# Optimization experiments

Measured on AMD Instinct MI355X. Metric: run time of the kernel, lower is better.

## Reference

```python
import jax, jax.numpy as jnp
import numpy as np

NUM_TOKEN = 16  # number of joint tokens; each locally-connected position has its own weights


def setup_inputs() -> dict:
    key = jax.random.key(0)
    k1, k2, k3 = jax.random.split(key, 3)
    b, n = 64, 256
    input_size, ff_size, output_size = 2048, 8192, 2048
    T = NUM_TOKEN
    cin, cff, cout = input_size // T, ff_size // T, output_size // T
    x = jax.random.normal(k1, (b, n, input_size), dtype=jnp.float32)
    # LocallyConnected2d weights: independent [out_ch, in_ch] matrix per token position t
    w1 = jax.random.normal(k2, (cff, cin, T), dtype=jnp.float32) * 0.05
    w2 = jax.random.normal(k3, (cout, cff, T), dtype=jnp.float32) * 0.05
    return {"x": x, "w1": w1, "w2": w2}


def reference(x, w1, w2):
    # x: [b, n, f]; reshape(b*n, f//T, T) matches torch's reshape(b*n, f//T, T, 1)
    b, n, f = x.shape
    T = NUM_TOKEN
    xr = x.reshape(b * n, f // T, T)  # [B, Cin, T]
    # LocallyConnected2d with k=1: per-position channel mixing (unfold degenerates to identity)
    h = jnp.einsum('bct,oct->bot', xr, w1)          # [B, Cff, T]
    h = jax.nn.gelu(h, approximate=False)           # nn.GELU default is exact erf form
    # dropout is identity in eval / deterministic reference
    y = jnp.einsum('bct,oct->bot', h, w2)           # [B, Cout, T]
    return y.reshape(b, n, -1)                      # feature index = o*T + t, same as torch
```

## Files before the change

kernel.cpp:

```cpp
#include <hip/hip_runtime.h>
#include <hip/hip_bf16.h>
#include <math.h>


typedef __attribute__((ext_vector_type(8))) short bf16x8;
typedef __attribute__((ext_vector_type(4))) float f32x4;

#define MFMA16(a,b,c) __builtin_amdgcn_mfma_f32_16x16x32_bf16((a),(b),(c),0,0,0)

#define N_ROWS   16384
#define XT_PLANE (16384*128)
#define W_TSTR   65536
#define W_JSTR   16384

static __device__ __forceinline__ unsigned short f2bf(float f){
  union{float f; unsigned u;} v; v.f = f;
  return (unsigned short)((v.u + 0x7FFFu + ((v.u>>16)&1u))>>16);
}
static __device__ __forceinline__ unsigned cvtpk(float lo, float hi){
  unsigned r;
  asm("v_cvt_pk_bf16_f32 %0, %1, %2" : "=v"(r) : "v"(lo), "v"(hi));
  return r;
}
static __device__ __forceinline__ float bflo(unsigned u){
  union{unsigned x; float f;} c; c.x = u<<16; return c.f;
}
static __device__ __forceinline__ float bfhi(unsigned u){
  union{unsigned x; float f;} c; c.x = u & 0xffff0000u; return c.f;
}
static __device__ __forceinline__ float gelu_fast(float x){
  float x2 = x*x;
  float m  = x*(-1.5957691216f - 0.0713548163f*x2);
  float e  = __expf(m);
  return x*__builtin_amdgcn_rcpf(1.0f + e);
}

typedef __attribute__((address_space(1))) const unsigned int gas_u32;
typedef __attribute__((address_space(3))) unsigned int las_u32;
static __device__ __forceinline__ void gload16(const void* g, void* l){
  __builtin_amdgcn_global_load_lds((gas_u32*)g, (las_u32*)l, 16, 0, 0);
}
static __device__ __forceinline__ unsigned lds_off(const void* p){
  return (unsigned)(size_t)(const __attribute__((address_space(3))) void*)p;
}

__global__ __launch_bounds__(256) void k_packw(const float* __restrict__ w1,
                                               const float* __restrict__ w2,
                                               unsigned short* __restrict__ w1p,
                                               unsigned short* __restrict__ w2p){
  int g = blockIdx.x*256 + threadIdx.x;
  bool is1 = (g < 131072);
  int gg = is1 ? g : (g - 131072);
  int l  = gg & 63, q = (l>>4), i = l & 15;
  int ks = (gg>>6)&3, m8 = (gg>>8)&7, jc = (gg>>11)&3, t = (gg>>13)&15;
  union { unsigned short s[8]; bf16x8 v; } u;
  if (is1){
    int o  = jc*128 + m8*16 + i;
    int c0 = ks*32 + q*8;
    #pragma unroll
    for (int j=0;j<8;++j) u.s[j] = f2bf(w1[(o*128 + c0 + j)*16 + t]);
    *(bf16x8*)(w1p + (size_t)gg*8) = u.v;
  } else {
    int o2  = m8*16 + i;
    int cf0 = jc*128 + ks*32 + q*8;
    #pragma unroll
    for (int j=0;j<8;++j) u.s[j] = f2bf(w2[(o2*512 + cf0 + j)*16 + t]);
    *(bf16x8*)(w2p + (size_t)gg*8) = u.v;
  }
}

#define TRRD(d, a, OFS) asm volatile("ds_read_b64_tr_b16 %0, %1 offset:" OFS \
                                     : "=v"(d) : "v"(a))
__global__ __launch_bounds__(256) void k_xt(const float* __restrict__ x,
                                            unsigned short* __restrict__ xt){
  __shared__ unsigned short ls[8*2048];
  const int r0 = blockIdx.x*8;
  const int tid = threadIdx.x;
  #pragma unroll
  for (int it=0; it<16; ++it){
    int idx = it*256 + tid;
    int row = idx>>9, rem = idx&511;
    float4 v = *(const float4*)(x + (size_t)(r0+row)*2048 + rem*4);
    unsigned lo = cvtpk(v.x, v.y), hi = cvtpk(v.z, v.w);
    unsigned long long p = ((unsigned long long)hi<<32) | lo;
    *(unsigned long long*)(ls + row*2048 + rem*4) = p;
  }
  __syncthreads();
  const int wv = tid>>6, l = tid&63, g = l>>4, i = l&15;
  unsigned base = lds_off(ls) + (unsigned)wv*8192u + (unsigned)l*8u;
  #pragma unroll
  for (int rr=0; rr<2; ++rr){
    unsigned long long d0,d1,d2,d3,d4,d5,d6,d7;
    if (rr==0){
      TRRD(d0, base, "0");    TRRD(d1, base, "512");
      TRRD(d2, base, "1024"); TRRD(d3, base, "1536");
      TRRD(d4, base, "2048"); TRRD(d5, base, "2560");
      TRRD(d6, base, "3072"); TRRD(d7, base, "3584");
    } else {
      TRRD(d0, base, "4096"); TRRD(d1, base, "4608");
      TRRD(d2, base, "5120"); TRRD(d3, base, "5632");
      TRRD(d4, base, "6144"); TRRD(d5, base, "6656");
      TRRD(d6, base, "7168"); TRRD(d7, base, "7680");
    }
    asm volatile("s_waitcnt lgkmcnt(0)" ::: "memory");
    __builtin_amdgcn_sched_barrier(0);
    unsigned short* xp = xt + (size_t)i*XT_PLANE
                       + (size_t)(r0 + 2*wv + rr)*128 + g*4;
    *(unsigned long long*)(xp + 0*16)  = d0;
    *(unsigned long long*)(xp + 1*16)  = d1;
    *(unsigned long long*)(xp + 2*16)  = d2;
    *(unsigned long long*)(xp + 3*16)  = d3;
    *(unsigned long long*)(xp + 4*16)  = d4;
    *(unsigned long long*)(xp + 5*16)  = d5;
    *(unsigned long long*)(xp + 6*16)  = d6;
    *(unsigned long long*)(xp + 7*16)  = d7;
  }
}

__global__ __launch_bounds__(256,2) void k_ffn(const unsigned short* __restrict__ xt,
                                               const unsigned short* __restrict__ w1p,
                                               const unsigned short* __restrict__ w2p,
                                               unsigned short* __restrict__ yt){
  __shared__ unsigned short ws[2*16384];
  const int bx = blockIdx.x;
  const int t = bx>>7, rt = bx&127, r0 = rt<<7;
  const int tid = threadIdx.x;
  const int wv = tid>>6, l = tid&63, q = l>>4, i = l&15;

  const unsigned short* w1t = w1p + (size_t)t*W_TSTR;
  const unsigned short* w2t = w2p + (size_t)t*W_TSTR;

  auto stage = [&](int hc, int buf){
    const int jc = hc>>1, half = hc&1;
    const unsigned short* w1c = w1t + jc*W_JSTR + half*8192;
    const unsigned short* w2c = w2t + jc*W_JSTR + half*1024;
    unsigned short* Wb = ws + buf*16384;
    #pragma unroll
    for (int c=0;c<8;++c){
      int k = wv*8 + c;
      if (k < 16){
        gload16(w1c + k*512 + l*8, Wb + k*512 + l*8);
      } else {
        int f = k - 16;
        gload16(w2c + (f>>1)*2048 + (f&1)*512 + l*8, Wb + 8192 + f*512 + l*8);
      }
    }
  };

  stage(0, 0);

  bf16x8 xb[4][2];
  {
    const unsigned short* xp = xt + (size_t)t*XT_PLANE + (size_t)(r0 + wv*32)*128;
    #pragma unroll
    for (int ks=0; ks<4; ++ks){
      xb[ks][0] = *(const bf16x8*)(xp + (size_t)i*128 + ks*32 + q*8);
      xb[ks][1] = *(const bf16x8*)(xp + (size_t)(i+16)*128 + ks*32 + q*8);
    }
  }
  __syncthreads();

  f32x4 accY[2][8];
  #pragma unroll
  for (int a=0;a<2;++a)
    #pragma unroll
    for (int b=0;b<8;++b) accY[a][b] = (f32x4){0.f,0.f,0.f,0.f};

  const int idxA = ((q&1)*32 + i)*4;
  const int idxB = idxA + 64;
  const int lo32 = (l < 32);

  int cur = 0;
  #pragma unroll 1
  for (int hc=0; hc<8; ++hc){
    if (hc < 7) stage(hc+1, cur^1);

    const unsigned short* W1 = ws + cur*16384;
    const unsigned short* W2 = W1 + 8192;

    f32x4 acc1[4][2];
    #pragma unroll
    for (int a=0;a<4;++a){ acc1[a][0]=(f32x4){0,0,0,0}; acc1[a][1]=(f32x4){0,0,0,0}; }
    #pragma unroll
    for (int ks=0; ks<4; ++ks){
      #pragma unroll
      for (int mt=0; mt<4; ++mt){
        bf16x8 af = *(const bf16x8*)(W1 + (mt*4+ks)*512 + l*8);
        acc1[mt][0] = MFMA16(af, xb[ks][0], acc1[mt][0]);
        acc1[mt][1] = MFMA16(af, xb[ks][1], acc1[mt][1]);
      }
    }

    unsigned pk[4][2][2];
    #pragma unroll
    for (int mt=0; mt<4; ++mt)
      #pragma unroll
      for (int nt=0; nt<2; ++nt){
        f32x4 v = acc1[mt][nt];
        pk[mt][nt][0] = cvtpk(gelu_fast(v.x), gelu_fast(v.y));
        pk[mt][nt][1] = cvtpk(gelu_fast(v.z), gelu_fast(v.w));
      }

    #pragma unroll
    for (int ks2=0; ks2<2; ++ks2){
      bf16x8 a2[2];
      #pragma unroll
      for (int nt=0; nt<2; ++nt){
        int pA0=(int)pk[2*ks2  ][nt][0], pA1=(int)pk[2*ks2  ][nt][1];
        int pB0=(int)pk[2*ks2+1][nt][0], pB1=(int)pk[2*ks2+1][nt][1];
        int a0 = __builtin_amdgcn_ds_bpermute(idxA, pA0);
        int b0 = __builtin_amdgcn_ds_bpermute(idxA, pB0);
        int a1 = __builtin_amdgcn_ds_bpermute(idxA, pA1);
        int b1 = __builtin_amdgcn_ds_bpermute(idxA, pB1);
        int a2r= __builtin_amdgcn_ds_bpermute(idxB, pA0);
        int b2 = __builtin_amdgcn_ds_bpermute(idxB, pB0);
        int a3 = __builtin_amdgcn_ds_bpermute(idxB, pA1);
        int b3 = __builtin_amdgcn_ds_bpermute(idxB, pB1);
        union{ int ii[4]; bf16x8 v; } u;
        u.ii[0] = lo32 ? a0 : b0;
        u.ii[1] = lo32 ? a1 : b1;
        u.ii[2] = lo32 ? a2r: b2;
        u.ii[3] = lo32 ? a3 : b3;
        a2[nt] = u.v;
      }
      #pragma unroll
      for (int nt2=0; nt2<8; ++nt2){
        bf16x8 bf = *(const bf16x8*)(W2 + (nt2*2+ks2)*512 + l*8);
        accY[0][nt2] = MFMA16(a2[0], bf, accY[0][nt2]);
        accY[1][nt2] = MFMA16(a2[1], bf, accY[1][nt2]);
      }
    }

    __syncthreads();
    cur ^= 1;
  }

  unsigned short* yp = yt + (size_t)t*XT_PLANE + (size_t)(r0 + wv*32)*128;
  #pragma unroll
  for (int mt2=0; mt2<2; ++mt2)
    #pragma unroll
    for (int nt2=0; nt2<8; ++nt2){
      f32x4 v = accY[mt2][nt2];
      unsigned p01 = cvtpk(v.x, v.y);
      unsigned p23 = cvtpk(v.z, v.w);
      int o = nt2*16 + i;
      int rowb = mt2*16 + q*4;
      yp[(rowb+0)*128 + o] = (unsigned short)(p01 & 0xffffu);
      yp[(rowb+1)*128 + o] = (unsigned short)(p01 >> 16);
      yp[(rowb+2)*128 + o] = (unsigned short)(p23 & 0xffffu);
      yp[(rowb+3)*128 + o] = (unsigned short)(p23 >> 16);
    }
}

__global__ __launch_bounds__(256) void k_out(const unsigned short* __restrict__ yt,
                                             float* __restrict__ out){
  const int r0 = blockIdx.x*8;
  const int tid = threadIdx.x;
  const int r = tid>>5, w = tid&31;
  const int og = w&15, tq0 = w>>4;
  #pragma unroll
  for (int it=0; it<2; ++it){
    int tq = tq0 + it*2;
    const unsigned short* yp = yt + (size_t)(tq*4)*XT_PLANE
                             + (size_t)(r0+r)*128 + og*8;
    union{ bf16x8 v; unsigned u[4]; } y0, y1, y2, y3;
    y0.v = *(const bf16x8*)(yp);
    y1.v = *(const bf16x8*)(yp + XT_PLANE);
    y2.v = *(const bf16x8*)(yp + 2*XT_PLANE);
    y3.v = *(const bf16x8*)(yp + 3*XT_PLANE);
    float* op = out + (size_t)(r0+r)*2048 + og*128 + tq*4;
    #pragma unroll
    for (int k=0;k<8;++k){
      unsigned w0 = y0.u[k>>1], w1 = y1.u[k>>1], w2 = y2.u[k>>1], w3 = y3.u[k>>1];
      f32x4 o4;
      if (k&1){ o4.x=bfhi(w0); o4.y=bfhi(w1); o4.z=bfhi(w2); o4.w=bfhi(w3); }
      else    { o4.x=bflo(w0); o4.y=bflo(w1); o4.z=bflo(w2); o4.w=bflo(w3); }
      *(f32x4*)(op + k*16) = o4;
    }
  }
}

__global__ __launch_bounds__(128) void k_naive(const float* __restrict__ x,
                                               const float* __restrict__ w1,
                                               const float* __restrict__ w2,
                                               float* __restrict__ out){
  int bid = blockIdx.x; int t = bid & 15; int row = bid >> 4;
  int tid = threadIdx.x;
  __shared__ float xsm[128]; __shared__ float hsm[512];
  xsm[tid] = x[(size_t)row*2048 + tid*16 + t];
  __syncthreads();
  for (int kk=0; kk<4; ++kk){
    int o = kk*128 + tid; float a = 0.f;
    for (int c=0;c<128;++c) a += xsm[c]*w1[(o*128+c)*16+t];
    hsm[o] = 0.5f*a*(1.0f+erff(a*0.70710678f));
  }
  __syncthreads();
  float a = 0.f;
  for (int cf=0; cf<512; ++cf) a += hsm[cf]*w2[(tid*512+cf)*16+t];
  out[(size_t)row*2048 + tid*16 + t] = a;
}

extern "C" void kernel_launch(void* const* d_in, const int* in_sizes, int n_in,
                              void* d_out, int out_size, void* d_ws, size_t ws_size,
                              hipStream_t stream){
  const float* x  = (const float*)d_in[0];
  const float* w1 = (const float*)d_in[1];
  const float* w2 = (const float*)d_in[2];
  float* out = (float*)d_out;

  const size_t NEEDED = 71303168ULL;
  if (ws_size < NEEDED || d_ws == nullptr){
    k_naive<<<dim3(16384*16), dim3(128), 0, stream>>>(x, w1, w2, out);
    return;
  }
  unsigned short* xt  = (unsigned short*)d_ws;
  unsigned short* w1p = xt + 33554432;
  unsigned short* w2p = w1p + 1048576;

  k_packw<<<dim3(1024), dim3(256), 0, stream>>>(w1, w2, w1p, w2p);
  k_xt  <<<dim3(2048), dim3(256), 0, stream>>>(x, xt);
  k_ffn <<<dim3(2048), dim3(256), 0, stream>>>(xt, w1p, w2p, xt);
  k_out <<<dim3(2048), dim3(256), 0, stream>>>(xt, out);
}
```

Before: 404.1 us.

## Coalesce transpose stores via LDS and shrink FFN weight stage for 3 blocks/CU

The x-transpose kernel now stages transposed data back through LDS, so it can write full 16-byte coalesced rows to the per-token planes instead of scattered 8-byte stores. The FFN kernel halves its per-iteration weight chunk (16 smaller stages instead of 8) and cuts LDS use so three blocks fit per CU. Its epilogue stages output through padded LDS before issuing vector stores. The output kernel now gathers the bf16 planes into LDS and uses transpose reads to write contiguous fp32 rows. The smaller FFN chunks mean more barriers and more stage overhead, traded against higher occupancy and better-coalesced global traffic.

```diff
diff --git a/kernel.cpp b/kernel.cpp
--- a/kernel.cpp
+++ b/kernel.cpp
@@ -22,11 +22,8 @@
   asm("v_cvt_pk_bf16_f32 %0, %1, %2" : "=v"(r) : "v"(lo), "v"(hi));
   return r;
 }
-static __device__ __forceinline__ float bflo(unsigned u){
-  union{unsigned x; float f;} c; c.x = u<<16; return c.f;
-}
-static __device__ __forceinline__ float bfhi(unsigned u){
-  union{unsigned x; float f;} c; c.x = u & 0xffff0000u; return c.f;
+static __device__ __forceinline__ float bfs(unsigned short s){
+  union{unsigned u; float f;} c; c.u = ((unsigned)s)<<16; return c.f;
 }
 static __device__ __forceinline__ float gelu_fast(float x){
   float x2 = x*x;
@@ -73,7 +70,7 @@
                                      : "=v"(d) : "v"(a))
 __global__ __launch_bounds__(256) void k_xt(const float* __restrict__ x,
                                             unsigned short* __restrict__ xt){
-  __shared__ unsigned short ls[8*2048];
+  __shared__ unsigned short ls[16512];
   const int r0 = blockIdx.x*8;
   const int tid = threadIdx.x;
   #pragma unroll
@@ -84,6 +81,191 @@
     unsigned lo = cvtpk(v.x, v.y), hi = cvtpk(v.z, v.w);
     unsigned long long p = ((unsigned long long)hi<<32) | lo;
     *(unsigned long long*)(ls + row*2048 + rem*4) = p;
+  }
+  __syncthreads();
+  const int wv = tid>>6, l = tid&63, g = l>>4, i = l&15;
+  unsigned base = lds_off(ls) + (unsigned)wv*8192u + (unsigned)l*8u;
+  unsigned long long d[16];
+  TRRD(d[0],  base, "0");    TRRD(d[1],  base, "512");
+  TRRD(d[2],  base, "1024"); TRRD(d[3],  base, "1536");
+  TRRD(d[4],  base, "2048"); TRRD(d[5],  base, "2560");
+  TRRD(d[6],  base, "3072"); TRRD(d[7],  base, "3584");
+  TRRD(d[8],  base, "4096"); TRRD(d[9],  base, "4608");
+  TRRD(d[10], base, "5120"); TRRD(d[11], base, "5632");
+  TRRD(d[12], base, "6144"); TRRD(d[13], base, "6656");
+  TRRD(d[14], base, "7168"); TRRD(d[15], base, "7680");
+  asm volatile("s_waitcnt lgkmcnt(0)" ::: "memory");
+  __builtin_amdgcn_sched_barrier(0);
+  __syncthreads();
+  #pragma unroll
+  for (int rr=0; rr<2; ++rr)
+    #pragma unroll
+    for (int ch=0; ch<8; ++ch)
+      *(unsigned long long*)(ls + i*1032 + (2*wv+rr)*128 + ch*16 + g*4) = d[rr*8+ch];
+  __syncthreads();
+  const int p = tid>>4, cg = tid&15;
+  #pragma unroll
+  for (int row=0; row<8; ++row){
+    bf16x8 v = *(const bf16x8*)(ls + p*1032 + row*128 + cg*8);
+    *(bf16x8*)(xt + (size_t)p*XT_PLANE + (size_t)(r0+row)*128 + cg*8) = v;
+  }
+}
+
+__global__ __launch_bounds__(256,3) void k_ffn(const unsigned short* __restrict__ xt,
+                                               const unsigned short* __restrict__ w1p,
+                                               const unsigned short* __restrict__ w2p,
+                                               unsigned short* __restrict__ yt){
+  __shared__ unsigned short ws[16896];
+  const int bx = blockIdx.x;
+  const int t = bx>>7, rt = bx&127, r0 = rt<<7;
+  const int tid = threadIdx.x;
+  const int wv = tid>>6, l = tid&63, q = l>>4, i = l&15;
+
+  const unsigned short* w1t = w1p + (size_t)t*W_TSTR;
+  const unsigned short* w2t = w2p + (size_t)t*W_TSTR;
+
+  auto stage = [&](int qc, int buf){
+    const int jc = qc>>2, q4 = qc&3;
+    const unsigned short* w1c = w1t + jc*W_JSTR;
+    const unsigned short* w2c = w2t + jc*W_JSTR;
+    unsigned short* Wb = ws + buf*8192;
+    #pragma unroll
+    for (int c=0;c<4;++c){
+      int k = wv*4 + c;
+      if (k < 8){
+        int m = k>>2, ks = k&3;
+        gload16(w1c + ((q4*2+m)*4+ks)*512 + l*8, Wb + (m*4+ks)*512 + l*8);
+      } else {
+        int f = k - 8;
+        gload16(w2c + (f*4+q4)*512 + l*8, Wb + 4096 + f*512 + l*8);
+      }
+    }
+  };
+
+  stage(0, 0);
+
+  bf16x8 xb[4][2];
+  {
+    const unsigned short* xp = xt + (size_t)t*XT_PLANE + (size_t)(r0 + wv*32)*128;
+    #pragma unroll
+    for (int ks=0; ks<4; ++ks){
+      xb[ks][0] = *(const bf16x8*)(xp + (size_t)i*128 + ks*32 + q*8);
+      xb[ks][1] = *(const bf16x8*)(xp + (size_t)(i+16)*128 + ks*32 + q*8);
+    }
+  }
+  __syncthreads();
+
+  f32x4 accY[2][8];
+  #pragma unroll
+  for (int a=0;a<2;++a)
+    #pragma unroll
+    for (int b=0;b<8;++b) accY[a][b] = (f32x4){0.f,0.f,0.f,0.f};
+
+  const int idxA = ((q&1)*32 + i)*4;
+  const int idxB = idxA + 64;
+  const int lo32 = (l < 32);
+
+  int cur = 0;
+  #pragma unroll 1
+  for (int qc=0; qc<16; ++qc){
+    if (qc < 15) stage(qc+1, cur^1);
+
+    const unsigned short* W1 = ws + cur*8192;
+    const unsigned short* W2 = W1 + 4096;
+
+    f32x4 acc1[2][2];
+    #pragma unroll
+    for (int a=0;a<2;++a){ acc1[a][0]=(f32x4){0,0,0,0}; acc1[a][1]=(f32x4){0,0,0,0}; }
+    #pragma unroll
+    for (int ks=0; ks<4; ++ks){
+      #pragma unroll
+      for (int m=0; m<2; ++m){
+        bf16x8 af = *(const bf16x8*)(W1 + (m*4+ks)*512 + l*8);
+        acc1[m][0] = MFMA16(af, xb[ks][0], acc1[m][0]);
+        acc1[m][1] = MFMA16(af, xb[ks][1], acc1[m][1]);
+      }
+    }
+
+    unsigned pk[2][2][2];
+    #pragma unroll
+    for (int m=0; m<2; ++m)
+      #pragma unroll
+      for (int nt=0; nt<2; ++nt){
+        f32x4 v = acc1[m][nt];
+        pk[m][nt][0] = cvtpk(gelu_fast(v.x), gelu_fast(v.y));
+        pk[m][nt][1] = cvtpk(gelu_fast(v.z), gelu_fast(v.w));
+      }
+
+    bf16x8 a2[2];
+    #pragma unroll
+    for (int nt=0; nt<2; ++nt){
+      int pA0=(int)pk[0][nt][0], pA1=(int)pk[0][nt][1];
+      int pB0=(int)pk[1][nt][0], pB1=(int)pk[1][nt][1];
+      int a0 = __builtin_amdgcn_ds_bpermute(idxA, pA0);
+      int b0 = __builtin_amdgcn_ds_bpermute(idxA, pB0);
+      int a1 = __builtin_amdgcn_ds_bpermute(idxA, pA1);
+      int b1 = __builtin_amdgcn_ds_bpermute(idxA, pB1);
+      int a2r= __builtin_amdgcn_ds_bpermute(idxB, pA0);
+      int b2 = __builtin_amdgcn_ds_bpermute(idxB, pB0);
+      int a3 = __builtin_amdgcn_ds_bpermute(idxB, pA1);
+      int b3 = __builtin_amdgcn_ds_bpermute(idxB, pB1);
+      union{ int ii[4]; bf16x8 v; } u;
+      u.ii[0] = lo32 ? a0 : b0;
+      u.ii[1] = lo32 ? a1 : b1;
+      u.ii[2] = lo32 ? a2r: b2;
+      u.ii[3] = lo32 ? a3 : b3;
+      a2[nt] = u.v;
+    }
+    #pragma unroll
+    for (int nt2=0; nt2<8; ++nt2){
+      bf16x8 bf = *(const bf16x8*)(W2 + nt2*512 + l*8);
+      accY[0][nt2] = MFMA16(a2[0], bf, accY[0][nt2]);
+      accY[1][nt2] = MFMA16(a2[1], bf, accY[1][nt2]);
+    }
+
+    __syncthreads();
+    cur ^= 1;
+  }
+
+  unsigned short* wse = ws + wv*4224;
+  #pragma unroll
+  for (int mt2=0; mt2<2; ++mt2)
+    #pragma unroll
+    for (int nt2=0; nt2<8; ++nt2){
+      f32x4 v = accY[mt2][nt2];
+      unsigned p01 = cvtpk(v.x, v.y), p23 = cvtpk(v.z, v.w);
+      int o = nt2*16 + i, rowb = mt2*16 + q*4;
+      wse[(rowb+0)*132 + o] = (unsigned short)(p01 & 0xffffu);
+      wse[(rowb+1)*132 + o] = (unsigned short)(p01 >> 16);
+      wse[(rowb+2)*132 + o] = (unsigned short)(p23 & 0xffffu);
+      wse[(rowb+3)*132 + o] = (unsigned short)(p23 >> 16);
+    }
+  asm volatile("s_waitcnt lgkmcnt(0)" ::: "memory");
+  __builtin_amdgcn_sched_barrier(0);
+  unsigned short* yp = yt + (size_t)t*XT_PLANE + (size_t)(r0 + wv*32)*128;
+  #pragma unroll
+  for (int u=0; u<8; ++u){
+    int row = u*4 + (l>>4);
+    int o8  = (l&15)*8;
+    bf16x8 vv = *(const bf16x8*)(wse + row*132 + o8);
+    *(bf16x8*)(yp + row*128 + o8) = vv;
+  }
+}
+
+__global__ __launch_bounds__(256) void k_out(const unsigned short* __restrict__ yt,
+                                             float* __restrict__ out){
+  __shared__ unsigned short ls[16384];
+  const int r0 = blockIdx.x*8;
+  const int tid = threadIdx.x;
+  {
+    const int tp = tid>>4, cg = tid&15;
+    const int og = cg>>1, o0 = (cg&1)*8;
+    #pragma unroll
+    for (int r=0; r<8; ++r){
+      bf16x8 v = *(const bf16x8*)(yt + (size_t)tp*XT_PLANE
+                                     + (size_t)(r0+r)*128 + cg*8);
+      *(bf16x8*)(ls + r*2048 + og*256 + tp*16 + o0) = v;
+    }
   }
   __syncthreads();
   const int wv = tid>>6, l = tid&63, g = l>>4, i = l&15;
@@ -104,178 +286,15 @@
     }
     asm volatile("s_waitcnt lgkmcnt(0)" ::: "memory");
     __builtin_amdgcn_sched_barrier(0);
-    unsigned short* xp = xt + (size_t)i*XT_PLANE
-                       + (size_t)(r0 + 2*wv + rr)*128 + g*4;
-    *(unsigned long long*)(xp + 0*16)  = d0;
-    *(unsigned long long*)(xp + 1*16)  = d1;
-    *(unsigned long long*)(xp + 2*16)  = d2;
-    *(unsigned long long*)(xp + 3*16)  = d3;
-    *(unsigned long long*)(xp + 4*16)  = d4;
-    *(unsigned long long*)(xp + 5*16)  = d5;
-    *(unsigned long long*)(xp + 6*16)  = d6;
-    *(unsigned long long*)(xp + 7*16)  = d7;
-  }
-}
-
-__global__ __launch_bounds__(256,2) void k_ffn(const unsigned short* __restrict__ xt,
-                                               const unsigned short* __restrict__ w1p,
-                                               const unsigned short* __restrict__ w2p,
-                                               unsigned short* __restrict__ yt){
-  __shared__ unsigned short ws[2*16384];
-  const int bx = blockIdx.x;
-  const int t = bx>>7, rt = bx&127, r0 = rt<<7;
-  const int tid = threadIdx.x;
-  const int wv = tid>>6, l = tid&63, q = l>>4, i = l&15;
-
-  const unsigned short* w1t = w1p + (size_t)t*W_TSTR;
-  const unsigned short* w2t = w2p + (size_t)t*W_TSTR;
-
-  auto stage = [&](int hc, int buf){
-    const int jc = hc>>1, half = hc&1;
-    const unsigned short* w1c = w1t + jc*W_JSTR + half*8192;
-    const unsigned short* w2c = w2t + jc*W_JSTR + half*1024;
-    unsigned short* Wb = ws + buf*16384;
-    #pragma unroll
-    for (int c=0;c<8;++c){
-      int k = wv*8 + c;
-      if (k < 16){
-        gload16(w1c + k*512 + l*8, Wb + k*512 + l*8);
-      } else {
-        int f = k - 16;
-        gload16(w2c + (f>>1)*2048 + (f&1)*512 + l*8, Wb + 8192 + f*512 + l*8);
-      }
-    }
-  };
-
-  stage(0, 0);
-
-  bf16x8 xb[4][2];
-  {
-    const unsigned short* xp = xt + (size_t)t*XT_PLANE + (size_t)(r0 + wv*32)*128;
-    #pragma unroll
-    for (int ks=0; ks<4; ++ks){
-      xb[ks][0] = *(const bf16x8*)(xp + (size_t)i*128 + ks*32 + q*8);
-      xb[ks][1] = *(const bf16x8*)(xp + (size_t)(i+16)*128 + ks*32 + q*8);
-    }
-  }
-  __syncthreads();
-
-  f32x4 accY[2][8];
-  #pragma unroll
-  for (int a=0;a<2;++a)
-    #pragma unroll
-    for (int b=0;b<8;++b) accY[a][b] = (f32x4){0.f,0.f,0.f,0.f};
-
-  const int idxA = ((q&1)*32 + i)*4;
-  const int idxB = idxA + 64;
-  const int lo32 = (l < 32);
-
-  int cur = 0;
-  #pragma unroll 1
-  for (int hc=0; hc<8; ++hc){
-    if (hc < 7) stage(hc+1, cur^1);
-
-    const unsigned short* W1 = ws + cur*16384;
-    const unsigned short* W2 = W1 + 8192;
-
-    f32x4 acc1[4][2];
-    #pragma unroll
-    for (int a=0;a<4;++a){ acc1[a][0]=(f32x4){0,0,0,0}; acc1[a][1]=(f32x4){0,0,0,0}; }
-    #pragma unroll
-    for (int ks=0; ks<4; ++ks){
-      #pragma unroll
-      for (int mt=0; mt<4; ++mt){
-        bf16x8 af = *(const bf16x8*)(W1 + (mt*4+ks)*512 + l*8);
-        acc1[mt][0] = MFMA16(af, xb[ks][0], acc1[mt][0]);
-        acc1[mt][1] = MFMA16(af, xb[ks][1], acc1[mt][1]);
-      }
-    }
-
-    unsigned pk[4][2][2];
-    #pragma unroll
-    for (int mt=0; mt<4; ++mt)
-      #pragma unroll
-      for (int nt=0; nt<2; ++nt){
-        f32x4 v = acc1[mt][nt];
-        pk[mt][nt][0] = cvtpk(gelu_fast(v.x), gelu_fast(v.y));
-        pk[mt][nt][1] = cvtpk(gelu_fast(v.z), gelu_fast(v.w));
-      }
-
-    #pragma unroll
-    for (int ks2=0; ks2<2; ++ks2){
-      bf16x8 a2[2];
-      #pragma unroll
-      for (int nt=0; nt<2; ++nt){
-        int pA0=(int)pk[2*ks2  ][nt][0], pA1=(int)pk[2*ks2  ][nt][1];
-        int pB0=(int)pk[2*ks2+1][nt][0], pB1=(int)pk[2*ks2+1][nt][1];
-        int a0 = __builtin_amdgcn_ds_bpermute(idxA, pA0);
-        int b0 = __builtin_amdgcn_ds_bpermute(idxA, pB0);
-        int a1 = __builtin_amdgcn_ds_bpermute(idxA, pA1);
-        int b1 = __builtin_amdgcn_ds_bpermute(idxA, pB1);
-        int a2r= __builtin_amdgcn_ds_bpermute(idxB, pA0);
-        int b2 = __builtin_amdgcn_ds_bpermute(idxB, pB0);
-        int a3 = __builtin_amdgcn_ds_bpermute(idxB, pA1);
-        int b3 = __builtin_amdgcn_ds_bpermute(idxB, pB1);
-        union{ int ii[4]; bf16x8 v; } u;
-        u.ii[0] = lo32 ? a0 : b0;
-        u.ii[1] = lo32 ? a1 : b1;
-        u.ii[2] = lo32 ? a2r: b2;
-        u.ii[3] = lo32 ? a3 : b3;
-        a2[nt] = u.v;
-      }
-      #pragma unroll
-      for (int nt2=0; nt2<8; ++nt2){
-        bf16x8 bf = *(const bf16x8*)(W2 + (nt2*2+ks2)*512 + l*8);
-        accY[0][nt2] = MFMA16(a2[0], bf, accY[0][nt2]);
-        accY[1][nt2] = MFMA16(a2[1], bf, accY[1][nt2]);
-      }
-    }
-
-    __syncthreads();
-    cur ^= 1;
-  }
-
-  unsigned short* yp = yt + (size_t)t*XT_PLANE + (size_t)(r0 + wv*32)*128;
-  #pragma unroll
-  for (int mt2=0; mt2<2; ++mt2)
-    #pragma unroll
-    for (int nt2=0; nt2<8; ++nt2){
-      f32x4 v = accY[mt2][nt2];
-      unsigned p01 = cvtpk(v.x, v.y);
-      unsigned p23 = cvtpk(v.z, v.w);
-      int o = nt2*16 + i;
-      int rowb = mt2*16 + q*4;
-      yp[(rowb+0)*128 + o] = (unsigned short)(p01 & 0xffffu);
-      yp[(rowb+1)*128 + o] = (unsigned short)(p01 >> 16);
-      yp[(rowb+2)*128 + o] = (unsigned short)(p23 & 0xffffu);
-      yp[(rowb+3)*128 + o] = (unsigned short)(p23 >> 16);
-    }
-}
-
-__global__ __launch_bounds__(256) void k_out(const unsigned short* __restrict__ yt,
-                                             float* __restrict__ out){
-  const int r0 = blockIdx.x*8;
-  const int tid = threadIdx.x;
-  const int r = tid>>5, w = tid&31;
-  const int og = w&15, tq0 = w>>4;
-  #pragma unroll
-  for (int it=0; it<2; ++it){
-    int tq = tq0 + it*2;
-    const unsigned short* yp = yt + (size_t)(tq*4)*XT_PLANE
-                             + (size_t)(r0+r)*128 + og*8;
-    union{ bf16x8 v; unsigned u[4]; } y0, y1, y2, y3;
-    y0.v = *(const bf16x8*)(yp);
-    y1.v = *(const bf16x8*)(yp + XT_PLANE);
-    y2.v = *(const bf16x8*)(yp + 2*XT_PLANE);
-    y3.v = *(const bf16x8*)(yp + 3*XT_PLANE);
-    float* op = out + (size_t)(r0+r)*2048 + og*128 + tq*4;
-    #pragma unroll
-    for (int k=0;k<8;++k){
-      unsigned w0 = y0.u[k>>1], w1 = y1.u[k>>1], w2 = y2.u[k>>1], w3 = y3.u[k>>1];
+    float* op = out + (size_t)(r0 + 2*wv + rr)*2048 + i*16 + g*4;
+    unsigned long long dd[8] = {d0,d1,d2,d3,d4,d5,d6,d7};
+    #pragma unroll
+    for (int og=0; og<8; ++og){
+      union{ unsigned long long u; unsigned short s[4]; } w; w.u = dd[og];
       f32x4 o4;
-      if (k&1){ o4.x=bfhi(w0); o4.y=bfhi(w1); o4.z=bfhi(w2); o4.w=bfhi(w3); }
-      else    { o4.x=bflo(w0); o4.y=bflo(w1); o4.z=bflo(w2); o4.w=bflo(w3); }
-      *(f32x4*)(op + k*16) = o4;
+      o4.x = bfs(w.s[0]); o4.y = bfs(w.s[1]);
+      o4.z = bfs(w.s[2]); o4.w = bfs(w.s[3]);
+      *(f32x4*)(op + og*256) = o4;
     }
   }
 }
```

New measurement: 369.6 us. 1.09x faster.
